# Kernel optimization log

Hardware: AMD Instinct MI355X
Metric: run time of the kernel (lower is better)

The kernel has to match this reference:

```python
import jax, jax.numpy as jnp
import numpy as np

# Module dims (match init_kwargs)
D_IN = 1024
N_PRI = 2048
D_PRI = 16
N_CLS = 25
D_CLS = 16
ITERS = 3
B = 64
EPS = 1e-6


def layer_norm(x, g, b, eps=1e-5):
    m = x.mean(-1, keepdims=True)
    v = ((x - m) ** 2).mean(-1, keepdims=True)
    return (x - m) / jnp.sqrt(v + eps) * g + b


def setup_inputs() -> dict:
    key = jax.random.key(0)
    ks = jax.random.split(key, 6)
    s = lambda n: 1.0 / np.sqrt(n)
    return {
        "z": jax.random.normal(ks[0], (B, D_IN), jnp.float32),
        # to_primary: Linear(d_in, n_primary*d_primary)
        "w1": jax.random.normal(ks[1], (D_IN, N_PRI * D_PRI), jnp.float32) * s(D_IN),
        "b1": jnp.zeros((N_PRI * D_PRI,), jnp.float32),
        # primary_act: LayerNorm(d_in) -> Linear(d_in, n_primary) -> Sigmoid
        "ln1_g": jnp.ones((D_IN,), jnp.float32),
        "ln1_b": jnp.zeros((D_IN,), jnp.float32),
        "w2": jax.random.normal(ks[2], (D_IN, N_PRI), jnp.float32) * s(D_IN),
        "b2": jnp.zeros((N_PRI,), jnp.float32),
        # CapsuleFC transform + EM routing params
        "w_caps": jax.random.normal(ks[3], (N_PRI, D_PRI, N_CLS, D_CLS), jnp.float32) * s(D_PRI),
        "beta_u": jnp.zeros((N_CLS,), jnp.float32),
        "beta_a": jnp.zeros((N_CLS,), jnp.float32),
        # to_logits: LayerNorm(d_class) -> Linear(d_class, 1)
        "ln2_g": jnp.ones((D_CLS,), jnp.float32),
        "ln2_b": jnp.zeros((D_CLS,), jnp.float32),
        "w3": jax.random.normal(ks[4], (D_CLS, 1), jnp.float32) * s(D_CLS),
        "b3": jnp.zeros((1,), jnp.float32),
    }


def em_routing(V, a_in, beta_u, beta_a, n_iter):
    # V: (b, n_in, n_out, d) votes; a_in: (b, n_in) primary activations
    b, n, o, d = V.shape
    R = jnp.full((b, n, o), 1.0 / o, V.dtype)  # routing assignments
    lam = jnp.asarray(1.0, V.dtype)            # inverse temperature
    for _ in range(n_iter):
        # M-step: weighted mean/variance per output capsule
        r = R * a_in[:, :, None]                                  # (b,n,o)
        r_sum = r.sum(axis=1) + EPS                               # (b,o)
        mu = jnp.einsum('bno,bnod->bod', r, V) / r_sum[..., None]  # (b,o,d)
        diff2 = (V - mu[:, None]) ** 2                            # (b,n,o,d)
        sigma2 = jnp.einsum('bno,bnod->bod', r, diff2) / r_sum[..., None] + EPS
        cost = (beta_u[None, :, None] + 0.5 * jnp.log(sigma2)) * r_sum[..., None]
        a_out = jax.nn.sigmoid(lam * (beta_a[None, :] - cost.sum(-1)))  # (b,o)
        # E-step: Gaussian log-likelihood of each vote under each output capsule
        logp = (-0.5 * (diff2 / sigma2[:, None]).sum(-1)
                - 0.5 * jnp.log(sigma2).sum(-1)[:, None, :])      # (b,n,o)
        R = jax.nn.softmax(jnp.log(a_out + EPS)[:, None, :] + logp, axis=-1)
    return mu, a_out, R


def reference(z, w1, b1, ln1_g, ln1_b, w2, b2, w_caps, beta_u, beta_a,
              ln2_g, ln2_b, w3, b3):
    b = z.shape[0]
    # primary poses (no squash: use_squash_primary=False)
    primary_pose = (z @ w1 + b1).reshape(b, N_PRI, D_PRI)
    # primary activations
    primary_act = jnp.clip(jax.nn.sigmoid(layer_norm(z, ln1_g, ln1_b) @ w2 + b2), 0.0, 1.0)
    # votes: each primary capsule predicts each class capsule's pose
    V = jnp.einsum('bni,niod->bnod', primary_pose, w_caps)  # (B, N_PRI, N_CLS, D_CLS)
    class_pose, class_act, q = em_routing(V, primary_act, beta_u, beta_a, ITERS)
    logits = (layer_norm(class_pose, ln2_g, ln2_b) @ w3 + b3).squeeze(-1)  # (B, N_CLS)
    acts = jnp.linalg.norm(class_pose, axis=-1)                            # (B, N_CLS)
    return logits, acts, class_pose, q
```

## Files before the change

kernel.cpp:

```cpp
#include <hip/hip_runtime.h>
#include <hip/hip_bf16.h>
#include <cstdio>

#define B     64
#define DIN   1024
#define NPRI  2048
#define DPRI  16
#define NCLS  25
#define DCLS  16
#define EMEPS 1e-6f
#define LNEPS 1e-5f
#define KS2   8
#define NCHUNK_S 16

#define OFF_POSE 0
#define OFF_ZN   (OFF_POSE + NPRI*DPRI*B)
#define OFF_ACTT (OFF_ZN + B*DIN)
#define OFF_G2P  (OFF_ACTT + NPRI*B)
#define OFF_V    (OFF_G2P + KS2*NPRI*B)
#define V_FLOATS (NPRI*NCLS*B*DCLS/2)
#define OFF_R    (OFF_V + V_FLOATS)
#define R_FLOATS (NPRI*NCLS*B/2)
#define OFF_PART (OFF_R + R_FLOATS)
#define OFF_STAT (OFF_PART + NCLS*NCHUNK_S*33*B)
#define OFF_MU   (OFF_STAT + NCLS*33*B)
#define OFF_MI4  (OFF_MU + NCLS*DCLS*B)
#define OFF_BASE (OFF_MI4 + NCLS*8*B*4)
#define OFF_ZH   (OFF_BASE + NCLS*B)
#define WS_FLOATS (OFF_ZH + B*DIN/2)

typedef __attribute__((ext_vector_type(8))) _Float16 f16x8;
typedef __attribute__((ext_vector_type(4))) float f32x4;

__device__ __forceinline__ unsigned pack_f16(float a, float b) {
  union { _Float16 h[2]; unsigned u; } x;
  x.h[0] = (_Float16)a; x.h[1] = (_Float16)b;
  return x.u;
}
__device__ __forceinline__ float f16lo(unsigned u) {
  union { unsigned u; _Float16 h[2]; } x; x.u = u; return (float)x.h[0];
}
__device__ __forceinline__ float f16hi(unsigned u) {
  union { unsigned u; _Float16 h[2]; } x; x.u = u; return (float)x.h[1];
}
__device__ __forceinline__ unsigned short f16bits(float a) {
  union { _Float16 h; unsigned short u; } x; x.h = (_Float16)a; return x.u;
}
__device__ __forceinline__ float f16val(unsigned short u) {
  union { unsigned short u; _Float16 h; } x; x.u = u; return (float)x.h;
}

__global__ __launch_bounds__(256) void k_zh(const float* __restrict__ z,
                                            unsigned* __restrict__ zh) {
  int idx = blockIdx.x * 256 + threadIdx.x;
  float2 v = ((const float2*)z)[idx];
  zh[idx] = pack_f16(v.x, v.y);
}

__global__ __launch_bounds__(256) void k_ln(const float* __restrict__ z,
                                            const float* __restrict__ g,
                                            const float* __restrict__ bb,
                                            float* __restrict__ zn) {
  int row = blockIdx.x, t = threadIdx.x;
  const float* zr = z + row * DIN;
  float4 v = ((const float4*)zr)[t];
  float s  = v.x + v.y + v.z + v.w;
  float s2 = v.x*v.x + v.y*v.y + v.z*v.z + v.w*v.w;
  for (int off = 32; off; off >>= 1) {
    s  += __shfl_down(s, off);
    s2 += __shfl_down(s2, off);
  }
  __shared__ float ls[8];
  int wv = t >> 6, ln = t & 63;
  if (ln == 0) { ls[wv*2] = s; ls[wv*2+1] = s2; }
  __syncthreads();
  s  = ls[0] + ls[2] + ls[4] + ls[6];
  s2 = ls[1] + ls[3] + ls[5] + ls[7];
  float mean = s * (1.0f / DIN);
  float var  = s2 * (1.0f / DIN) - mean * mean;
  float inv  = 1.0f / sqrtf(var + LNEPS);
  float4 gg = ((const float4*)g)[t];
  float4 bv = ((const float4*)bb)[t];
  float4 o;
  o.x = (v.x - mean) * inv * gg.x + bv.x;
  o.y = (v.y - mean) * inv * gg.y + bv.y;
  o.z = (v.z - mean) * inv * gg.z + bv.z;
  o.w = (v.w - mean) * inv * gg.w + bv.w;
  ((float4*)(zn + row * DIN))[t] = o;
}

__global__ __launch_bounds__(256) void k_gemm1m(const unsigned* __restrict__ zh,
                                                const float* __restrict__ w1,
                                                const float* __restrict__ b1,
                                                float* __restrict__ poseT) {
  __shared__ __align__(16) unsigned bt[64 * 68];
  int t = threadIdx.x;
  int c0 = blockIdx.x * 64;
  int l = t & 63, w = t >> 6;
  int colw = w * 16 + (l & 15);
  int kq = l >> 4;

  f32x4 acc0 = {0,0,0,0}, acc1 = {0,0,0,0}, acc2 = {0,0,0,0}, acc3 = {0,0,0,0};

  int sc = t & 63;
  int kp0 = t >> 6;

  for (int kc = 0; kc < 8; ++kc) {
    int k0 = kc * 128;
    __syncthreads();
#pragma unroll
    for (int i = 0; i < 16; ++i) {
      int kp = kp0 + 4 * i;
      int k = k0 + 2 * kp;
      float v0 = w1[(size_t)k * 32768 + c0 + sc];
      float v1 = w1[(size_t)(k + 1) * 32768 + c0 + sc];
      bt[sc * 68 + kp] = pack_f16(v0, v1);
    }
    __syncthreads();
#pragma unroll
    for (int ks = 0; ks < 4; ++ks) {
      union { uint4 u; f16x8 h; } bc_;
      bc_.u = *(const uint4*)&bt[colw * 68 + ks * 16 + kq * 4];
#pragma unroll
      for (int rc = 0; rc < 4; ++rc) {
        int row = rc * 16 + (l & 15);
        union { uint4 u; f16x8 h; } ac_;
        ac_.u = *(const uint4*)&zh[((size_t)row * DIN + k0 + ks * 32 + kq * 8) >> 1];
        if (rc == 0) acc0 = __builtin_amdgcn_mfma_f32_16x16x32_f16(ac_.h, bc_.h, acc0, 0, 0, 0);
        if (rc == 1) acc1 = __builtin_amdgcn_mfma_f32_16x16x32_f16(ac_.h, bc_.h, acc1, 0, 0, 0);
        if (rc == 2) acc2 = __builtin_amdgcn_mfma_f32_16x16x32_f16(ac_.h, bc_.h, acc2, 0, 0, 0);
        if (rc == 3) acc3 = __builtin_amdgcn_mfma_f32_16x16x32_f16(ac_.h, bc_.h, acc3, 0, 0, 0);
      }
    }
  }
  int c = c0 + colw;
  float bc = b1[c];
  float* pdst = poseT + (size_t)c * 64 + kq * 4;
  {
    float4 o = {acc0[0] + bc, acc0[1] + bc, acc0[2] + bc, acc0[3] + bc};
    *(float4*)&pdst[0] = o;
  }
  {
    float4 o = {acc1[0] + bc, acc1[1] + bc, acc1[2] + bc, acc1[3] + bc};
    *(float4*)&pdst[16] = o;
  }
  {
    float4 o = {acc2[0] + bc, acc2[1] + bc, acc2[2] + bc, acc2[3] + bc};
    *(float4*)&pdst[32] = o;
  }
  {
    float4 o = {acc3[0] + bc, acc3[1] + bc, acc3[2] + bc, acc3[3] + bc};
    *(float4*)&pdst[48] = o;
  }
}

__global__ __launch_bounds__(256, 2) void k_gemm2p(const float* __restrict__ zn,
                                                   const float* __restrict__ w2,
                                                   float* __restrict__ part) {
  __shared__ __align__(16) float znT[128 * 68];
  __shared__ __align__(16) float wl[128 * 68];
  int t = threadIdx.x;
  int c0 = blockIdx.x * 64;
  int k0 = blockIdx.y * 128;
  int zr_ = t >> 2, za = t & 3;
  int wk = t >> 1, wc = (t & 1) * 32;

#pragma unroll
  for (int jj = 0; jj < 4; ++jj) {
    int kb = za * 8 + jj * 32;
    const float* src = zn + zr_ * DIN + k0 + kb;
    float4 v0 = *(const float4*)src;
    float4 v1 = *(const float4*)(src + 4);
    znT[(kb+0)*68 + zr_] = v0.x; znT[(kb+1)*68 + zr_] = v0.y;
    znT[(kb+2)*68 + zr_] = v0.z; znT[(kb+3)*68 + zr_] = v0.w;
    znT[(kb+4)*68 + zr_] = v1.x; znT[(kb+5)*68 + zr_] = v1.y;
    znT[(kb+6)*68 + zr_] = v1.z; znT[(kb+7)*68 + zr_] = v1.w;
  }
  const float* wsrc = w2 + (size_t)(k0 + wk) * NPRI + c0 + wc;
#pragma unroll
  for (int j = 0; j < 8; ++j)
    *(float4*)&wl[wk * 68 + wc + j * 4] = *(const float4*)(wsrc + j * 4);
  __syncthreads();

  int r0 = (t >> 4) * 4, c0l = (t & 15) * 4;
  float acc[4][4];
#pragma unroll
  for (int j = 0; j < 4; ++j)
#pragma unroll
    for (int i = 0; i < 4; ++i) acc[j][i] = 0.f;

#pragma unroll 4
  for (int k = 0; k < 128; ++k) {
    float4 z4 = *(const float4*)&znT[k * 68 + r0];
    float4 w4 = *(const float4*)&wl[k * 68 + c0l];
    float zz[4] = {z4.x, z4.y, z4.z, z4.w};
    float ww[4] = {w4.x, w4.y, w4.z, w4.w};
#pragma unroll
    for (int j = 0; j < 4; ++j)
#pragma unroll
      for (int i = 0; i < 4; ++i) acc[j][i] += ww[j] * zz[i];
  }
  float* pdst = part + ((size_t)blockIdx.y * NPRI + c0 + c0l) * 64 + r0;
#pragma unroll
  for (int j = 0; j < 4; ++j) {
    float4 o = {acc[j][0], acc[j][1], acc[j][2], acc[j][3]};
    *(float4*)&pdst[j * 64] = o;
  }
}

__global__ __launch_bounds__(256) void k_gemm2r(const float* __restrict__ part,
                                                const float* __restrict__ b2,
                                                float* __restrict__ actt) {
  int idx = blockIdx.x * 256 + threadIdx.x;
  float4 s = {0.f, 0.f, 0.f, 0.f};
#pragma unroll
  for (int kz = 0; kz < KS2; ++kz) {
    float4 v = *(const float4*)&part[(size_t)kz * NPRI * 64 + idx * 4];
    s.x += v.x; s.y += v.y; s.z += v.z; s.w += v.w;
  }
  int c = (idx * 4) >> 6;
  float bc = b2[c];
  float4 o;
  o.x = fminf(fmaxf(1.0f / (1.0f + expf(-(s.x + bc))), 0.0f), 1.0f);
  o.y = fminf(fmaxf(1.0f / (1.0f + expf(-(s.y + bc))), 0.0f), 1.0f);
  o.z = fminf(fmaxf(1.0f / (1.0f + expf(-(s.z + bc))), 0.0f), 1.0f);
  o.w = fminf(fmaxf(1.0f / (1.0f + expf(-(s.w + bc))), 0.0f), 1.0f);
  *(float4*)&actt[idx * 4] = o;
}

__global__ __launch_bounds__(256) void k_votes(const float* __restrict__ poseT,
                                               const float* __restrict__ wcaps,
                                               unsigned* __restrict__ V) {
  __shared__ __align__(16) float wl[6400];
  __shared__ __align__(16) float pl[64 * 16];
  int n = blockIdx.x, t = threadIdx.x;
  const float* wsrc = wcaps + (size_t)n * 6400;
  for (int idx = t * 4; idx < 6400; idx += 1024)
    *(float4*)(wl + idx) = *(const float4*)(wsrc + idx);
  {
    float4 v = *(const float4*)(poseT + n * 1024 + t * 4);
    int i = (t * 4) >> 6, b = (t * 4) & 63;
    pl[(b+0)*16 + i] = v.x; pl[(b+1)*16 + i] = v.y;
    pl[(b+2)*16 + i] = v.z; pl[(b+3)*16 + i] = v.w;
  }
  __syncthreads();
  if (t >= 200) return;
  int o = t / 8, d0 = (t % 8) * 2;
  float w0[16], w1_[16];
#pragma unroll
  for (int i = 0; i < 16; ++i) {
    w0[i]  = wl[(i * 25 + o) * 16 + d0];
    w1_[i] = wl[(i * 25 + o) * 16 + d0 + 1];
  }
  unsigned* vd = V + (((size_t)n * 25 + o) * 64 * 16 + d0) / 2;
  for (int b = 0; b < 64; ++b) {
    const float* pb = &pl[b * 16];
    float a0 = 0.f, a1 = 0.f;
#pragma unroll
    for (int i = 0; i < 16; ++i) {
      float p = pb[i];
      a0 += p * w0[i];
      a1 += p * w1_[i];
    }
    vd[b * 8] = pack_f16(a0, a1);
  }
}

template <bool UNIFORM>
__global__ __launch_bounds__(256) void k_stats(const unsigned* __restrict__ V,
                                               const float* __restrict__ actt,
                                               const unsigned short* __restrict__ Rh,
                                               float* __restrict__ part) {
  int o = blockIdx.y;
  int t = threadIdx.x, b = t & 63, wv = t >> 6;
  float S0 = 0.f, S1[16], S2[16];
#pragma unroll
  for (int d = 0; d < 16; ++d) { S1[d] = 0.f; S2[d] = 0.f; }
  int n0 = blockIdx.x * 128 + wv * 32;
  for (int k = 0; k < 32; ++k) {
    int n = n0 + k;
    float a = actt[n * 64 + b];
    float r = UNIFORM ? a * (1.0f / 25.0f)
                      : f16val(Rh[((size_t)n * 25 + o) * 64 + b]) * a;
    const uint4* vp = (const uint4*)(V + (((size_t)n * 25 + o) * 64 + b) * 8);
    uint4 u0 = vp[0], u1 = vp[1];
    unsigned uu[8] = {u0.x, u0.y, u0.z, u0.w, u1.x, u1.y, u1.z, u1.w};
    S0 += r;
#pragma unroll
    for (int q = 0; q < 8; ++q) {
      float v0 = f16lo(uu[q]), v1 = f16hi(uu[q]);
      float t0 = r * v0, t1 = r * v1;
      S1[2*q]   += t0;          S1[2*q+1] += t1;
      S2[2*q]   += t0 * v0;     S2[2*q+1] += t1 * v1;
    }
  }
  __shared__ float red[4 * 33 * 64];
  red[(wv * 33 + 0) * 64 + b] = S0;
#pragma unroll
  for (int d = 0; d < 16; ++d) {
    red[(wv * 33 + 1 + d) * 64 + b]  = S1[d];
    red[(wv * 33 + 17 + d) * 64 + b] = S2[d];
  }
  __syncthreads();
  if (wv == 0) {
    for (int s = 0; s < 33; ++s) {
      float tot = red[s * 64 + b] + red[(33 + s) * 64 + b] +
                  red[(66 + s) * 64 + b] + red[(99 + s) * 64 + b];
      part[((o * NCHUNK_S + blockIdx.x) * 33 + s) * 64 + b] = tot;
    }
  }
}

__global__ __launch_bounds__(256) void k_reduce(const float* __restrict__ part,
                                                float* __restrict__ stats) {
  int o = blockIdx.x;
  for (int idx = threadIdx.x; idx < 33 * 64; idx += 256) {
    float s = 0.f;
#pragma unroll
    for (int c = 0; c < NCHUNK_S; ++c)
      s += part[(o * NCHUNK_S + c) * 33 * 64 + idx];
    stats[o * 33 * 64 + idx] = s;
  }
}

__global__ __launch_bounds__(64) void k_finish(const float* __restrict__ stats,
                                               const float* __restrict__ beta_u,
                                               const float* __restrict__ beta_a,
                                               float* __restrict__ mu,
                                               float* __restrict__ mi4,
                                               float* __restrict__ basew) {
  int o = blockIdx.x, b = threadIdx.x;
  const float* st = stats + o * 33 * 64;
  float s0 = st[b];
  float rs = s0 + EMEPS;
  float inv_rs = 1.0f / rs;
  float ldet = 0.f;
  float mloc[16], iloc[16];
#pragma unroll
  for (int d = 0; d < 16; ++d) {
    float s1 = st[(1 + d) * 64 + b];
    float s2 = st[(17 + d) * 64 + b];
    float m = s1 * inv_rs;
    float var = (s2 - 2.0f * m * s1 + m * m * s0) * inv_rs;
    float sg = fmaxf(var, 0.0f) + EMEPS;
    mloc[d] = m;
    iloc[d] = 1.0f / sg;
    mu[(o * 16 + d) * 64 + b] = m;
    ldet += logf(sg);
  }
#pragma unroll
  for (int q = 0; q < 8; ++q) {
    float4 v = {mloc[2*q], iloc[2*q], mloc[2*q+1], iloc[2*q+1]};
    *(float4*)&mi4[((o * 8 + q) * 64 + b) * 4] = v;
  }
  float cost = (16.0f * beta_u[o] + 0.5f * ldet) * rs;
  float x = beta_a[o] - cost;
  float a = 1.0f / (1.0f + expf(-x));
  basew[o * 64 + b] = logf(a + EMEPS) - 0.5f * ldet;
}

template <bool FINAL>
__global__ __launch_bounds__(256) void k_estep(const unsigned* __restrict__ V,
                                               const float* __restrict__ mi4,
                                               const float* __restrict__ basew,
                                               unsigned short* __restrict__ Rh,
                                               float* __restrict__ qout) {
  int t = threadIdx.x, b = t & 63, ng = t >> 6;
  int n = blockIdx.x * 4 + ng;
  float l[25];
  float mx = -1e30f;
#pragma unroll
  for (int o = 0; o < 25; ++o) {
    const uint4* vp = (const uint4*)(V + (((size_t)n * 25 + o) * 64 + b) * 8);
    uint4 u0 = vp[0], u1 = vp[1];
    unsigned uu[8] = {u0.x, u0.y, u0.z, u0.w, u1.x, u1.y, u1.z, u1.w};
    float acc = 0.f;
#pragma unroll
    for (int qq = 0; qq < 8; ++qq) {
      float4 mi = *(const float4*)&mi4[((o * 8 + qq) * 64 + b) * 4];
      float d0 = f16lo(uu[qq]) - mi.x;
      float d1 = f16hi(uu[qq]) - mi.z;
      acc += d0 * d0 * mi.y + d1 * d1 * mi.w;
    }
    l[o] = basew[o * 64 + b] - 0.5f * acc;
    mx = fmaxf(mx, l[o]);
  }
  float s = 0.f;
#pragma unroll
  for (int o = 0; o < 25; ++o) { l[o] = expf(l[o] - mx); s += l[o]; }
  float inv = 1.0f / s;
  if (FINAL) {
    float* qp = qout + ((size_t)b * NPRI + n) * 25;
#pragma unroll
    for (int o = 0; o < 25; ++o) qp[o] = l[o] * inv;
  } else {
#pragma unroll
    for (int o = 0; o < 25; ++o)
      Rh[((size_t)n * 25 + o) * 64 + b] = f16bits(l[o] * inv);
  }
}

__global__ __launch_bounds__(64) void k_out(const float* __restrict__ mu,
                                            const float* __restrict__ g2,
                                            const float* __restrict__ bb2,
                                            const float* __restrict__ w3,
                                            const float* __restrict__ b3,
                                            float* __restrict__ out) {
  int o = blockIdx.x, b = threadIdx.x;
  float m[16];
  float s = 0.f;
#pragma unroll
  for (int d = 0; d < 16; ++d) { m[d] = mu[(o * 16 + d) * 64 + b]; s += m[d]; }
  float mean = s * (1.0f / 16.0f);
  float var = 0.f;
#pragma unroll
  for (int d = 0; d < 16; ++d) { float dd = m[d] - mean; var += dd * dd; }
  var *= (1.0f / 16.0f);
  float inv = 1.0f / sqrtf(var + LNEPS);
  float logit = 0.f, nrm = 0.f;
#pragma unroll
  for (int d = 0; d < 16; ++d) {
    float nh = (m[d] - mean) * inv * g2[d] + bb2[d];
    logit += nh * w3[d];
    nrm += m[d] * m[d];
  }
  out[b * 25 + o] = logit + b3[0];
  out[1600 + b * 25 + o] = sqrtf(nrm);
  float* pp = out + 3200 + (b * 25 + o) * 16;
#pragma unroll
  for (int d = 0; d < 16; ++d) pp[d] = m[d];
}

extern "C" void kernel_launch(void* const* d_in, const int* in_sizes, int n_in,
                              void* d_out, int out_size, void* d_ws, size_t ws_size,
                              hipStream_t stream) {
  const float* z      = (const float*)d_in[0];
  const float* w1     = (const float*)d_in[1];
  const float* b1     = (const float*)d_in[2];
  const float* ln1g   = (const float*)d_in[3];
  const float* ln1b   = (const float*)d_in[4];
  const float* w2     = (const float*)d_in[5];
  const float* b2     = (const float*)d_in[6];
  const float* wcaps  = (const float*)d_in[7];
  const float* beta_u = (const float*)d_in[8];
  const float* beta_a = (const float*)d_in[9];
  const float* ln2g   = (const float*)d_in[10];
  const float* ln2b   = (const float*)d_in[11];
  const float* w3     = (const float*)d_in[12];
  const float* b3     = (const float*)d_in[13];

  if (ws_size < (size_t)WS_FLOATS * 4) {
    fprintf(stderr, "kernel_launch: ws too small: %zu < %zu bytes\n",
            ws_size, (size_t)WS_FLOATS * 4);
  }

  float* ws    = (float*)d_ws;
  float* out   = (float*)d_out;
  float* poseT = ws + OFF_POSE;
  float* zn    = ws + OFF_ZN;
  float* actt  = ws + OFF_ACTT;
  float* g2p   = ws + OFF_G2P;
  unsigned* V  = (unsigned*)(ws + OFF_V);
  unsigned short* Rh = (unsigned short*)(ws + OFF_R);
  float* part  = ws + OFF_PART;
  float* st    = ws + OFF_STAT;
  float* muw   = ws + OFF_MU;
  float* mi4   = ws + OFF_MI4;
  float* bse   = ws + OFF_BASE;
  unsigned* zh = (unsigned*)(ws + OFF_ZH);

  k_zh<<<128, 256, 0, stream>>>(z, zh);
  k_ln<<<64, 256, 0, stream>>>(z, ln1g, ln1b, zn);
  k_gemm1m<<<512, 256, 0, stream>>>(zh, w1, b1, poseT);
  k_gemm2p<<<dim3(32, KS2), 256, 0, stream>>>(zn, w2, g2p);
  k_gemm2r<<<128, 256, 0, stream>>>(g2p, b2, actt);
  k_votes<<<2048, 256, 0, stream>>>(poseT, wcaps, V);

  k_stats<true><<<dim3(NCHUNK_S, 25), 256, 0, stream>>>(V, actt, Rh, part);
  k_reduce<<<25, 256, 0, stream>>>(part, st);
  k_finish<<<25, 64, 0, stream>>>(st, beta_u, beta_a, muw, mi4, bse);

  for (int it = 0; it < 2; ++it) {
    k_estep<false><<<512, 256, 0, stream>>>(V, mi4, bse, Rh, nullptr);
    k_stats<false><<<dim3(NCHUNK_S, 25), 256, 0, stream>>>(V, actt, Rh, part);
    k_reduce<<<25, 256, 0, stream>>>(part, st);
    k_finish<<<25, 64, 0, stream>>>(st, beta_u, beta_a, muw, mi4, bse);
  }

  k_estep<true><<<512, 256, 0, stream>>>(V, mi4, bse, nullptr, out + 28800);
  k_out<<<25, 64, 0, stream>>>(muw, ln2g, ln2b, w3, b3, out);
}
```

Baseline: 422.6 us.

## Split K across two wave groups in gemm1 with LDS-staged A and vectorized loads

The first GEMM now runs 512 threads per block. Two halves of the block each handle half of the K dimension into separate LDS buffers, and their partial accumulators are reduced through shared memory at the end. The activation tile is now staged in LDS instead of being reloaded from global memory for every MFMA. The w1 loads become float4 to coalesce the global reads. The aim is more parallelism in flight per block to hide latency on this memory-bound w1 read, at the cost of more LDS use and an extra reduction step.

```diff
diff --git a/kernel.cpp b/kernel.cpp
--- a/kernel.cpp
+++ b/kernel.cpp
@@ -89,68 +89,87 @@
   ((float4*)(zn + row * DIN))[t] = o;
 }
 
-__global__ __launch_bounds__(256) void k_gemm1m(const unsigned* __restrict__ zh,
+__global__ __launch_bounds__(512) void k_gemm1m(const unsigned* __restrict__ zh,
                                                 const float* __restrict__ w1,
                                                 const float* __restrict__ b1,
                                                 float* __restrict__ poseT) {
-  __shared__ __align__(16) unsigned bt[64 * 68];
+  __shared__ __align__(16) unsigned bt[2][64 * 68];
+  __shared__ __align__(16) unsigned zl[2][64 * 68];
   int t = threadIdx.x;
   int c0 = blockIdx.x * 64;
   int l = t & 63, w = t >> 6;
-  int colw = w * 16 + (l & 15);
-  int kq = l >> 4;
+  int kh = w >> 2, cw = w & 3;
+  int c15 = l & 15, kq = l >> 4;
+  int h  = t >> 8;
+  int th = t & 255;
+  int s_kp = th >> 2;
+  int s_q  = th & 3;
 
   f32x4 acc0 = {0,0,0,0}, acc1 = {0,0,0,0}, acc2 = {0,0,0,0}, acc3 = {0,0,0,0};
 
-  int sc = t & 63;
-  int kp0 = t >> 6;
-
-  for (int kc = 0; kc < 8; ++kc) {
-    int k0 = kc * 128;
+  for (int it = 0; it < 4; ++it) {
+    int k0 = (h * 4 + it) * 128;
+#pragma unroll
+    for (int u = 0; u < 4; ++u) {
+      int cq = s_q + 4 * u;
+      const float* src0 = w1 + (size_t)(k0 + 2 * s_kp) * 32768 + c0 + cq * 4;
+      float4 r0 = *(const float4*)src0;
+      float4 r1 = *(const float4*)(src0 + 32768);
+      unsigned* dst = &bt[h][(cq * 4) * 68 + s_kp];
+      dst[0]   = pack_f16(r0.x, r1.x);
+      dst[68]  = pack_f16(r0.y, r1.y);
+      dst[136] = pack_f16(r0.z, r1.z);
+      dst[204] = pack_f16(r0.w, r1.w);
+    }
+#pragma unroll
+    for (int u = 0; u < 4; ++u) {
+      int ku4 = s_q + 4 * u;
+      uint4 v = *(const uint4*)&zh[(size_t)s_kp * 512 + (k0 >> 1) + ku4 * 4];
+      *(uint4*)&zl[h][s_kp * 68 + ku4 * 4] = v;
+    }
     __syncthreads();
 #pragma unroll
-    for (int i = 0; i < 16; ++i) {
-      int kp = kp0 + 4 * i;
-      int k = k0 + 2 * kp;
-      float v0 = w1[(size_t)k * 32768 + c0 + sc];
-      float v1 = w1[(size_t)(k + 1) * 32768 + c0 + sc];
-      bt[sc * 68 + kp] = pack_f16(v0, v1);
+    for (int ks = 0; ks < 4; ++ks) {
+      union { uint4 u; f16x8 hh; } bf, a0, a1, a2, a3;
+      bf.u = *(const uint4*)&bt[kh][(cw * 16 + c15) * 68 + ks * 16 + kq * 4];
+      a0.u = *(const uint4*)&zl[kh][(c15)      * 68 + ks * 16 + kq * 4];
+      a1.u = *(const uint4*)&zl[kh][(16 + c15) * 68 + ks * 16 + kq * 4];
+      a2.u = *(const uint4*)&zl[kh][(32 + c15) * 68 + ks * 16 + kq * 4];
+      a3.u = *(const uint4*)&zl[kh][(48 + c15) * 68 + ks * 16 + kq * 4];
+      acc0 = __builtin_amdgcn_mfma_f32_16x16x32_f16(a0.hh, bf.hh, acc0, 0, 0, 0);
+      acc1 = __builtin_amdgcn_mfma_f32_16x16x32_f16(a1.hh, bf.hh, acc1, 0, 0, 0);
+      acc2 = __builtin_amdgcn_mfma_f32_16x16x32_f16(a2.hh, bf.hh, acc2, 0, 0, 0);
+      acc3 = __builtin_amdgcn_mfma_f32_16x16x32_f16(a3.hh, bf.hh, acc3, 0, 0, 0);
     }
     __syncthreads();
-#pragma unroll
-    for (int ks = 0; ks < 4; ++ks) {
-      union { uint4 u; f16x8 h; } bc_;
-      bc_.u = *(const uint4*)&bt[colw * 68 + ks * 16 + kq * 4];
-#pragma unroll
-      for (int rc = 0; rc < 4; ++rc) {
-        int row = rc * 16 + (l & 15);
-        union { uint4 u; f16x8 h; } ac_;
-        ac_.u = *(const uint4*)&zh[((size_t)row * DIN + k0 + ks * 32 + kq * 8) >> 1];
-        if (rc == 0) acc0 = __builtin_amdgcn_mfma_f32_16x16x32_f16(ac_.h, bc_.h, acc0, 0, 0, 0);
-        if (rc == 1) acc1 = __builtin_amdgcn_mfma_f32_16x16x32_f16(ac_.h, bc_.h, acc1, 0, 0, 0);
-        if (rc == 2) acc2 = __builtin_amdgcn_mfma_f32_16x16x32_f16(ac_.h, bc_.h, acc2, 0, 0, 0);
-        if (rc == 3) acc3 = __builtin_amdgcn_mfma_f32_16x16x32_f16(ac_.h, bc_.h, acc3, 0, 0, 0);
-      }
-    }
-  }
-  int c = c0 + colw;
-  float bc = b1[c];
-  float* pdst = poseT + (size_t)c * 64 + kq * 4;
-  {
-    float4 o = {acc0[0] + bc, acc0[1] + bc, acc0[2] + bc, acc0[3] + bc};
-    *(float4*)&pdst[0] = o;
-  }
-  {
-    float4 o = {acc1[0] + bc, acc1[1] + bc, acc1[2] + bc, acc1[3] + bc};
-    *(float4*)&pdst[16] = o;
-  }
-  {
-    float4 o = {acc2[0] + bc, acc2[1] + bc, acc2[2] + bc, acc2[3] + bc};
-    *(float4*)&pdst[32] = o;
-  }
-  {
-    float4 o = {acc3[0] + bc, acc3[1] + bc, acc3[2] + bc, acc3[3] + bc};
-    *(float4*)&pdst[48] = o;
+  }
+
+  float* red = (float*)&zl[0][0];
+  if (kh == 1) {
+    int cc = cw * 16 + c15;
+    *(float4*)&red[cc * 68 + kq * 4]      = *(float4*)&acc0;
+    *(float4*)&red[cc * 68 + 16 + kq * 4] = *(float4*)&acc1;
+    *(float4*)&red[cc * 68 + 32 + kq * 4] = *(float4*)&acc2;
+    *(float4*)&red[cc * 68 + 48 + kq * 4] = *(float4*)&acc3;
+  }
+  __syncthreads();
+  if (kh == 0) {
+    int cc = cw * 16 + c15;
+    int c = c0 + cc;
+    float bc = b1[c];
+    float4 r0 = *(float4*)&red[cc * 68 + kq * 4];
+    float4 r1 = *(float4*)&red[cc * 68 + 16 + kq * 4];
+    float4 r2 = *(float4*)&red[cc * 68 + 32 + kq * 4];
+    float4 r3 = *(float4*)&red[cc * 68 + 48 + kq * 4];
+    float* pdst = poseT + (size_t)c * 64 + kq * 4;
+    float4 o0 = {acc0[0] + r0.x + bc, acc0[1] + r0.y + bc, acc0[2] + r0.z + bc, acc0[3] + r0.w + bc};
+    float4 o1 = {acc1[0] + r1.x + bc, acc1[1] + r1.y + bc, acc1[2] + r1.z + bc, acc1[3] + r1.w + bc};
+    float4 o2 = {acc2[0] + r2.x + bc, acc2[1] + r2.y + bc, acc2[2] + r2.z + bc, acc2[3] + r2.w + bc};
+    float4 o3 = {acc3[0] + r3.x + bc, acc3[1] + r3.y + bc, acc3[2] + r3.z + bc, acc3[3] + r3.w + bc};
+    *(float4*)&pdst[0]  = o0;
+    *(float4*)&pdst[16] = o1;
+    *(float4*)&pdst[32] = o2;
+    *(float4*)&pdst[48] = o3;
   }
 }
 
@@ -471,7 +490,7 @@
 
   k_zh<<<128, 256, 0, stream>>>(z, zh);
   k_ln<<<64, 256, 0, stream>>>(z, ln1g, ln1b, zn);
-  k_gemm1m<<<512, 256, 0, stream>>>(zh, w1, b1, poseT);
+  k_gemm1m<<<512, 512, 0, stream>>>(zh, w1, b1, poseT);
   k_gemm2p<<<dim3(32, KS2), 256, 0, stream>>>(zn, w2, g2p);
   k_gemm2r<<<128, 256, 0, stream>>>(g2p, b2, actt);
   k_votes<<<2048, 256, 0, stream>>>(poseT, wcaps, V);
```

New measurement: 357.9 us. 1.18x faster.
